# Kernel optimization log

Hardware: AMD Instinct MI355X
Metric: run time of the kernel (lower is better)

## Reference

```python
import jax, jax.numpy as jnp
import numpy as np
import math

EMBED_DIM = 128
NUM_HEADS = 16
HEAD_DIM = EMBED_DIM // NUM_HEADS  # = 8 = n_wires of the quantum circuit


def setup_inputs() -> dict:
    key = jax.random.key(0)
    k1, k2, k3 = jax.random.split(key, 3)
    B, S = 4, 2048
    x = jax.random.normal(k1, (B, S, EMBED_DIM), dtype=jnp.float32)
    # shared trainable RX angles of the single q_layer (applied to every head)
    theta = jax.random.normal(k2, (HEAD_DIM,), dtype=jnp.float32)
    w_out = jax.random.normal(k3, (EMBED_DIM, EMBED_DIM), dtype=jnp.float32) / math.sqrt(EMBED_DIM)
    mask = jnp.ones((B, S), dtype=jnp.int32)
    return {"x": x, "theta": theta, "w_out": w_out, "mask": mask}


def quantum_linear(x_head, theta):
    # Circuit: RX(x_i) encode + RX(theta_i) on wire i, CNOT chain (i, i+1),
    # then <Z_j>. For product state |psi_i> = RX(phi_i)|0>, <Z_i> = cos(phi_i),
    # and the CNOT chain gives final <Z_j> = prod_{i<=j} cos(phi_i).
    phi = x_head + theta  # [..., D] broadcast over leading dims
    return jnp.cumprod(jnp.cos(phi), axis=-1)


def reference(x, theta, w_out, mask):
    B, S, E = x.shape
    H, D = NUM_HEADS, HEAD_DIM
    xs = x.reshape(B, S, H, D)
    q = quantum_linear(xs, theta).transpose(0, 2, 1, 3)  # [B, H, S, D]; k = v = q
    scores = jnp.einsum("bhsd,bhtd->bhst", q, q) / math.sqrt(D)
    scores = jnp.where(mask[:, None, None, :] == 0, -1e9, scores)
    probs = jax.nn.softmax(scores, axis=-1)  # dropout is identity in eval
    attn = jnp.einsum("bhst,bhtd->bhsd", probs, q)
    attn = attn.transpose(0, 2, 1, 3).reshape(B, S, E)
    return attn @ w_out.T
```

## Files before the change

kernel.cpp:

```cpp
#include <hip/hip_runtime.h>
#include <hip/hip_bf16.h>
#include <hip/hip_fp16.h>

#define NB 4
#define NS 2048
#define NE 128
#define NH 16
#define ND 8

#define THALF 1024
#define NCH 32
#define VSTRIDE 1032

typedef __attribute__((ext_vector_type(8))) _Float16 half8;
typedef __attribute__((ext_vector_type(4))) float f32x4;

__device__ __forceinline__ unsigned int pkrtz(float a, float b) {
    typedef __fp16 fp16v2 __attribute__((ext_vector_type(2)));
    union { fp16v2 h; unsigned int u; } v;
    v.h = __builtin_amdgcn_cvt_pkrtz(a, b);
    return v.u;
}
__device__ __forceinline__ unsigned short f2h(float a) {
    return __half_as_ushort(__float2half(a));
}
__device__ __forceinline__ half8 mk_half8(unsigned u0, unsigned u1,
                                          unsigned u2, unsigned u3) {
    union { half8 h; unsigned u[4]; } v;
    v.u[0] = u0; v.u[1] = u1; v.u[2] = u2; v.u[3] = u3;
    return v.h;
}

__device__ __forceinline__ void qrow(const float* __restrict__ xp,
                                     const float* th, float* p) {
    float4 a = *(const float4*)xp, c = *(const float4*)(xp + 4);
    float t = 1.f;
    t *= cosf(a.x + th[0]); p[0] = t;
    t *= cosf(a.y + th[1]); p[1] = t;
    t *= cosf(a.z + th[2]); p[2] = t;
    t *= cosf(a.w + th[3]); p[3] = t;
    t *= cosf(c.x + th[4]); p[4] = t;
    t *= cosf(c.y + th[5]); p[5] = t;
    t *= cosf(c.z + th[6]); p[6] = t;
    t *= cosf(c.w + th[7]); p[7] = t;
}

__global__ __launch_bounds__(512, 6) void attn_kernel(
        const float* __restrict__ x,
        const float* __restrict__ theta,
        const int* __restrict__ mask,
        unsigned short* __restrict__ mid) {
    __shared__ unsigned short qhl[THALF * ND + 24];
    __shared__ unsigned short vT[9 * VSTRIDE];

    const int bid = blockIdx.x;
    const int bh = bid >> 3;
    const int b = bh >> 4, h = bh & (NH - 1);
    const int meighth = bid & 7;
    const int tid = threadIdx.x;

    const float SC = 0.71421629f;

    float th[ND];
#pragma unroll
    for (int d = 0; d < ND; d++) th[d] = theta[d];

    const int wave = tid >> 6, lane = tid & 63;
    const int quad = lane >> 4, l15 = lane & 15;
    const int mbase = meighth * 256 + wave * 32;
    const int bph = meighth >> 2;
    const int lmb = (meighth & 3) * 256 + wave * 32;

    if (tid < 24) qhl[THALF * ND + tid] = 0;

    half8 hz = {0, 0, 0, 0, 0, 0, 0, 0};
    half8 bm0 = hz, bm1 = hz;

    const int vrow = (l15 < 9) ? l15 : 8;
    const unsigned short* vbase = &vT[vrow * VSTRIDE];

    f32x4 O0 = {0.f, 0.f, 0.f, 0.f}, O1 = {0.f, 0.f, 0.f, 0.f};
    const f32x4 zc = {0.f, 0.f, 0.f, 0.f};

    for (int p = 0; p < 2; p++) {
        const int tph = bph ^ p;
        {
            int chs = tid >> 4, i = tid & 15;
            int ta = 4 * (i >> 2) + 2 * (i & 1) + 16 * ((i >> 1) & 1);
            int r0 = chs * 32 + ta, r1 = r0 + 1;
            int g0 = tph * THALF + r0;
            float p0[ND], p1[ND];
            qrow(x + ((size_t)(b * NS + g0) * NE + h * ND), th, p0);
            qrow(x + ((size_t)(b * NS + g0 + 1) * NE + h * ND), th, p1);
            float mz0 = mask[b * NS + g0] ? 1.f : 0.f;
            float mz1 = mask[b * NS + g0 + 1] ? 1.f : 0.f;
            uint4 qa, qb;
            qa.x = pkrtz(p0[0] * SC, p0[1] * SC);
            qa.y = pkrtz(p0[2] * SC, p0[3] * SC);
            qa.z = pkrtz(p0[4] * SC, p0[5] * SC);
            qa.w = pkrtz(p0[6] * SC, p0[7] * SC);
            qb.x = pkrtz(p1[0] * SC, p1[1] * SC);
            qb.y = pkrtz(p1[2] * SC, p1[3] * SC);
            qb.z = pkrtz(p1[4] * SC, p1[5] * SC);
            qb.w = pkrtz(p1[6] * SC, p1[7] * SC);
            *(uint4*)&qhl[r0 * ND] = qa;
            *(uint4*)&qhl[r1 * ND] = qb;
#pragma unroll
            for (int d = 0; d < ND; d++)
                *(unsigned int*)&vT[d * VSTRIDE + chs * 32 + 2 * i] =
                    pkrtz(p0[d] * mz0, p1[d] * mz1);
            *(unsigned int*)&vT[8 * VSTRIDE + chs * 32 + 2 * i] = pkrtz(mz0, mz1);
        }
        __syncthreads();

        if (p == 0) {
            bm0 = quad ? hz : *(const half8*)&qhl[(lmb + l15) * ND];
            bm1 = quad ? hz : *(const half8*)&qhl[(lmb + 16 + l15) * ND];
        }

        for (int ch = 0; ch < NCH; ch++) {
            int tb = ch * 32;
            half8 at0 = *(const half8*)&qhl[(tb + l15) * ND + quad * 8];
            half8 at1 = *(const half8*)&qhl[(tb + 16 + l15) * ND + quad * 8];
            half8 vf  = *(const half8*)&vbase[tb + quad * 8];

            f32x4 s00 = __builtin_amdgcn_mfma_f32_16x16x32_f16(at0, bm0, zc, 0, 0, 0);
            f32x4 s01 = __builtin_amdgcn_mfma_f32_16x16x32_f16(at0, bm1, zc, 0, 0, 0);
            f32x4 s10 = __builtin_amdgcn_mfma_f32_16x16x32_f16(at1, bm0, zc, 0, 0, 0);
            f32x4 s11 = __builtin_amdgcn_mfma_f32_16x16x32_f16(at1, bm1, zc, 0, 0, 0);

            half8 pA0 = mk_half8(
                pkrtz(__builtin_amdgcn_exp2f(s00[0]), __builtin_amdgcn_exp2f(s00[1])),
                pkrtz(__builtin_amdgcn_exp2f(s00[2]), __builtin_amdgcn_exp2f(s00[3])),
                pkrtz(__builtin_amdgcn_exp2f(s10[0]), __builtin_amdgcn_exp2f(s10[1])),
                pkrtz(__builtin_amdgcn_exp2f(s10[2]), __builtin_amdgcn_exp2f(s10[3])));
            half8 pA1 = mk_half8(
                pkrtz(__builtin_amdgcn_exp2f(s01[0]), __builtin_amdgcn_exp2f(s01[1])),
                pkrtz(__builtin_amdgcn_exp2f(s01[2]), __builtin_amdgcn_exp2f(s01[3])),
                pkrtz(__builtin_amdgcn_exp2f(s11[0]), __builtin_amdgcn_exp2f(s11[1])),
                pkrtz(__builtin_amdgcn_exp2f(s11[2]), __builtin_amdgcn_exp2f(s11[3])));

            O0 = __builtin_amdgcn_mfma_f32_16x16x32_f16(pA0, vf, O0, 0, 0, 0);
            O1 = __builtin_amdgcn_mfma_f32_16x16x32_f16(pA1, vf, O1, 0, 0, 0);
        }
        __syncthreads();
    }

#pragma unroll
    for (int mt = 0; mt < 2; mt++) {
        f32x4 O = mt ? O1 : O0;
#pragma unroll
        for (int r = 0; r < 4; r++) {
            float lsum = __shfl(O[r], (lane & 48) | 8, 64);
            float v = O[r] / lsum;
            if (l15 < ND) {
                int m = mbase + mt * 16 + quad * 4 + r;
                mid[(size_t)(b * NS + m) * NE + h * ND + l15] = f2h(v);
            }
        }
    }
}

__global__ __launch_bounds__(256) void proj_kernel(
        const unsigned short* __restrict__ mid,
        const float* __restrict__ w,
        float* __restrict__ out) {
    __shared__ unsigned short wf[NE * 136];
    __shared__ unsigned short am[32 * 136];
    const int rb = blockIdx.x * 32;
    const int tid = threadIdx.x;

    for (int i = tid; i < 2048; i += 256) {
        const float* wp = w + i * 8;
        float4 a = *(const float4*)wp, c = *(const float4*)(wp + 4);
        uint4 pk;
        pk.x = pkrtz(a.x, a.y); pk.y = pkrtz(a.z, a.w);
        pk.z = pkrtz(c.x, c.y); pk.w = pkrtz(c.z, c.w);
        int n = i >> 4, k8 = (i & 15) * 8;
        *(uint4*)&wf[n * 136 + k8] = pk;
    }
    for (int i = tid; i < 512; i += 256) {
        int r = i >> 4, k8 = (i & 15) * 8;
        uint4 v = *(const uint4*)&mid[(size_t)(rb + r) * NE + k8];
        *(uint4*)&am[r * 136 + k8] = v;
    }
    __syncthreads();

    const int wave = tid >> 6, lane = tid & 63;
    const int quad = lane >> 4, l15 = lane & 15;
    const int mt = wave & 1, nh = wave >> 1;

    half8 af[4];
#pragma unroll
    for (int kt = 0; kt < 4; kt++)
        af[kt] = *(const half8*)&am[(mt * 16 + l15) * 136 + kt * 32 + quad * 8];

#pragma unroll
    for (int nt = 0; nt < 4; nt++) {
        int n0 = (nh * 4 + nt) * 16;
        f32x4 acc = {0.f, 0.f, 0.f, 0.f};
#pragma unroll
        for (int kt = 0; kt < 4; kt++) {
            half8 bf = *(const half8*)&wf[(n0 + l15) * 136 + kt * 32 + quad * 8];
            acc = __builtin_amdgcn_mfma_f32_16x16x32_f16(af[kt], bf, acc, 0, 0, 0);
        }
#pragma unroll
        for (int r = 0; r < 4; r++)
            out[(size_t)(rb + mt * 16 + quad * 4 + r) * NE + n0 + l15] = acc[r];
    }
}

extern "C" void kernel_launch(void* const* d_in, const int* in_sizes, int n_in,
                              void* d_out, int out_size, void* d_ws, size_t ws_size,
                              hipStream_t stream) {
    const float* x     = (const float*)d_in[0];
    const float* theta = (const float*)d_in[1];
    const float* w_out = (const float*)d_in[2];
    const int*   mask  = (const int*)d_in[3];
    float* out = (float*)d_out;

    unsigned short* mid16 = (unsigned short*)d_ws;

    attn_kernel<<<NB * NH * 8, 512, 0, stream>>>(x, theta, mask, mid16);
    proj_kernel<<<NB * NS / 32, 256, 0, stream>>>(mid16, w_out, out);
}
```

Measured before the change: 106.2 us.

## Precompute Q/V in separate kernel and use 16x16x16 MFMA for scores

Moves the cosine-cumprod Q computation and the transposed, masked V layout out of the attention kernel into a new qgen kernel that writes fp16 Q and V^T to workspace. Each of the 8 attention blocks per head previously recomputed Q for all 2048 keys, and now they only copy precomputed tiles into LDS. The score MFMA also switches from 16x16x32 with zero-padded K to 16x16x16 on half4 operands, halving the wasted K work. This adds an extra kernel launch and a global round trip for Q/V, and drops the occupancy hint from the launch bounds.

```diff
diff --git a/kernel.cpp b/kernel.cpp
--- a/kernel.cpp
+++ b/kernel.cpp
@@ -11,8 +11,10 @@
 #define THALF 1024
 #define NCH 32
 #define VSTRIDE 1032
+#define VGSTR 2056
 
 typedef __attribute__((ext_vector_type(8))) _Float16 half8;
+typedef __attribute__((ext_vector_type(4))) _Float16 half4;
 typedef __attribute__((ext_vector_type(4))) float f32x4;
 
 __device__ __forceinline__ unsigned int pkrtz(float a, float b) {
@@ -45,10 +47,56 @@
     t *= cosf(c.w + th[7]); p[7] = t;
 }
 
-__global__ __launch_bounds__(512, 6) void attn_kernel(
+__global__ __launch_bounds__(256) void qgen_kernel(
         const float* __restrict__ x,
         const float* __restrict__ theta,
         const int* __restrict__ mask,
+        unsigned short* __restrict__ qg,
+        unsigned short* __restrict__ vtg) {
+    const int gid = blockIdx.x * 256 + threadIdx.x;
+    const int b = gid >> 14;
+    const int h = gid & (NH - 1);
+    const int j = (gid >> 4) & 1023;
+    const int s0 = 2 * j;
+    const float SC = 0.71421629f;
+
+    float th[ND];
+#pragma unroll
+    for (int d = 0; d < ND; d++) th[d] = theta[d];
+
+    float p0[ND], p1[ND];
+    qrow(x + ((size_t)(b * NS + s0) * NE + h * ND), th, p0);
+    qrow(x + ((size_t)(b * NS + s0 + 1) * NE + h * ND), th, p1);
+    const float mz0 = mask[b * NS + s0] ? 1.f : 0.f;
+    const float mz1 = mask[b * NS + s0 + 1] ? 1.f : 0.f;
+    const int bh = b * NH + h;
+
+    uint4 qa, qb;
+    qa.x = pkrtz(p0[0] * SC, p0[1] * SC);
+    qa.y = pkrtz(p0[2] * SC, p0[3] * SC);
+    qa.z = pkrtz(p0[4] * SC, p0[5] * SC);
+    qa.w = pkrtz(p0[6] * SC, p0[7] * SC);
+    qb.x = pkrtz(p1[0] * SC, p1[1] * SC);
+    qb.y = pkrtz(p1[2] * SC, p1[3] * SC);
+    qb.z = pkrtz(p1[4] * SC, p1[5] * SC);
+    qb.w = pkrtz(p1[6] * SC, p1[7] * SC);
+    *(uint4*)&qg[((size_t)bh * NS + s0) * ND] = qa;
+    *(uint4*)&qg[((size_t)bh * NS + s0 + 1) * ND] = qb;
+
+    const int H = s0 >> 10, r0 = s0 & 1023;
+    const int chs = r0 >> 5, u = (r0 & 31) >> 1;
+    const int i = (u & 1) | (((u >> 3) & 1) << 1) | (((u >> 1) & 3) << 2);
+    const int col = H * THALF + chs * 32 + 2 * i;
+    unsigned short* vb = vtg + (size_t)bh * 9 * VGSTR + col;
+#pragma unroll
+    for (int d = 0; d < ND; d++)
+        *(unsigned int*)&vb[d * VGSTR] = pkrtz(p0[d] * mz0, p1[d] * mz1);
+    *(unsigned int*)&vb[8 * VGSTR] = pkrtz(mz0, mz1);
+}
+
+__global__ __launch_bounds__(512) void attn_kernel(
+        const unsigned short* __restrict__ qg,
+        const unsigned short* __restrict__ vtg,
         unsigned short* __restrict__ mid) {
     __shared__ unsigned short qhl[THALF * ND + 24];
     __shared__ unsigned short vT[9 * VSTRIDE];
@@ -59,22 +107,17 @@
     const int meighth = bid & 7;
     const int tid = threadIdx.x;
 
-    const float SC = 0.71421629f;
-
-    float th[ND];
-#pragma unroll
-    for (int d = 0; d < ND; d++) th[d] = theta[d];
-
     const int wave = tid >> 6, lane = tid & 63;
     const int quad = lane >> 4, l15 = lane & 15;
     const int mbase = meighth * 256 + wave * 32;
-    const int bph = meighth >> 2;
-    const int lmb = (meighth & 3) * 256 + wave * 32;
 
     if (tid < 24) qhl[THALF * ND + tid] = 0;
 
-    half8 hz = {0, 0, 0, 0, 0, 0, 0, 0};
-    half8 bm0 = hz, bm1 = hz;
+    half4 hz4 = {0, 0, 0, 0};
+    const unsigned short* qmrow = qg + ((size_t)bh * NS + mbase + l15) * ND
+                                + (quad < 2 ? quad * 4 : 0);
+    half4 bm0 = (quad < 2) ? *(const half4*)qmrow : hz4;
+    half4 bm1 = (quad < 2) ? *(const half4*)(qmrow + 16 * ND) : hz4;
 
     const int vrow = (l15 < 9) ? l15 : 8;
     const unsigned short* vbase = &vT[vrow * VSTRIDE];
@@ -83,51 +126,31 @@
     const f32x4 zc = {0.f, 0.f, 0.f, 0.f};
 
     for (int p = 0; p < 2; p++) {
-        const int tph = bph ^ p;
         {
-            int chs = tid >> 4, i = tid & 15;
-            int ta = 4 * (i >> 2) + 2 * (i & 1) + 16 * ((i >> 1) & 1);
-            int r0 = chs * 32 + ta, r1 = r0 + 1;
-            int g0 = tph * THALF + r0;
-            float p0[ND], p1[ND];
-            qrow(x + ((size_t)(b * NS + g0) * NE + h * ND), th, p0);
-            qrow(x + ((size_t)(b * NS + g0 + 1) * NE + h * ND), th, p1);
-            float mz0 = mask[b * NS + g0] ? 1.f : 0.f;
-            float mz1 = mask[b * NS + g0 + 1] ? 1.f : 0.f;
-            uint4 qa, qb;
-            qa.x = pkrtz(p0[0] * SC, p0[1] * SC);
-            qa.y = pkrtz(p0[2] * SC, p0[3] * SC);
-            qa.z = pkrtz(p0[4] * SC, p0[5] * SC);
-            qa.w = pkrtz(p0[6] * SC, p0[7] * SC);
-            qb.x = pkrtz(p1[0] * SC, p1[1] * SC);
-            qb.y = pkrtz(p1[2] * SC, p1[3] * SC);
-            qb.z = pkrtz(p1[4] * SC, p1[5] * SC);
-            qb.w = pkrtz(p1[6] * SC, p1[7] * SC);
-            *(uint4*)&qhl[r0 * ND] = qa;
-            *(uint4*)&qhl[r1 * ND] = qb;
-#pragma unroll
-            for (int d = 0; d < ND; d++)
-                *(unsigned int*)&vT[d * VSTRIDE + chs * 32 + 2 * i] =
-                    pkrtz(p0[d] * mz0, p1[d] * mz1);
-            *(unsigned int*)&vT[8 * VSTRIDE + chs * 32 + 2 * i] = pkrtz(mz0, mz1);
+            const uint4* qs = (const uint4*)(qg + ((size_t)bh * NS + p * THALF) * ND);
+            uint4* qd = (uint4*)qhl;
+            qd[tid] = qs[tid];
+            qd[tid + 512] = qs[tid + 512];
+        }
+        {
+            const unsigned short* vs = vtg + (size_t)bh * 9 * VGSTR + p * THALF;
+            for (int jj = tid; jj < 1152; jj += 512) {
+                int d = jj >> 7, c = (jj & 127) << 3;
+                *(uint4*)&vT[d * VSTRIDE + c] = *(const uint4*)&vs[d * VGSTR + c];
+            }
         }
         __syncthreads();
-
-        if (p == 0) {
-            bm0 = quad ? hz : *(const half8*)&qhl[(lmb + l15) * ND];
-            bm1 = quad ? hz : *(const half8*)&qhl[(lmb + 16 + l15) * ND];
-        }
 
         for (int ch = 0; ch < NCH; ch++) {
             int tb = ch * 32;
-            half8 at0 = *(const half8*)&qhl[(tb + l15) * ND + quad * 8];
-            half8 at1 = *(const half8*)&qhl[(tb + 16 + l15) * ND + quad * 8];
+            half4 at0 = *(const half4*)&qhl[(tb + l15) * ND + quad * 4];
+            half4 at1 = *(const half4*)&qhl[(tb + 16 + l15) * ND + quad * 4];
             half8 vf  = *(const half8*)&vbase[tb + quad * 8];
 
-            f32x4 s00 = __builtin_amdgcn_mfma_f32_16x16x32_f16(at0, bm0, zc, 0, 0, 0);
-            f32x4 s01 = __builtin_amdgcn_mfma_f32_16x16x32_f16(at0, bm1, zc, 0, 0, 0);
-            f32x4 s10 = __builtin_amdgcn_mfma_f32_16x16x32_f16(at1, bm0, zc, 0, 0, 0);
-            f32x4 s11 = __builtin_amdgcn_mfma_f32_16x16x32_f16(at1, bm1, zc, 0, 0, 0);
+            f32x4 s00 = __builtin_amdgcn_mfma_f32_16x16x16f16(at0, bm0, zc, 0, 0, 0);
+            f32x4 s01 = __builtin_amdgcn_mfma_f32_16x16x16f16(at0, bm1, zc, 0, 0, 0);
+            f32x4 s10 = __builtin_amdgcn_mfma_f32_16x16x16f16(at1, bm0, zc, 0, 0, 0);
+            f32x4 s11 = __builtin_amdgcn_mfma_f32_16x16x16f16(at1, bm1, zc, 0, 0, 0);
 
             half8 pA0 = mk_half8(
                 pkrtz(__builtin_amdgcn_exp2f(s00[0]), __builtin_amdgcn_exp2f(s00[1])),
@@ -220,7 +243,10 @@
     float* out = (float*)d_out;
 
     unsigned short* mid16 = (unsigned short*)d_ws;
-
-    attn_kernel<<<NB * NH * 8, 512, 0, stream>>>(x, theta, mask, mid16);
+    unsigned short* qg  = mid16 + (size_t)NB * NS * NE;
+    unsigned short* vtg = qg + (size_t)NB * NH * NS * ND;
+
+    qgen_kernel<<<NB * NH * NS / 2 / 256, 256, 0, stream>>>(x, theta, mask, qg, vtg);
+    attn_kernel<<<NB * NH * 8, 512, 0, stream>>>(qg, vtg, mid16);
     proj_kernel<<<NB * NS / 32, 256, 0, stream>>>(mid16, w_out, out);
 }
```

Result: faster. 103.8 us (-2.3%).
